# Kernel optimization log

Measured on AMD Instinct MI355X. Metric: run time of the kernel, lower is better.

Reference implementation:

```python
import jax, jax.numpy as jnp
import numpy as np

B, S, HID, NH = 2, 2048, 2048, 16
NOPE, ROPE, VD = 128, 64, 128
QKD = NOPE + ROPE          # 192
KVR, QR = 512, 1536
EPS = 1e-6
SCALE = QKD ** (-0.5)


def rmsnorm(x, gamma, eps=EPS):
    return x * jax.lax.rsqrt(jnp.mean(x * x, axis=-1, keepdims=True) + eps) * gamma


def rotate_half(x):
    h = x.shape[-1] // 2
    return jnp.concatenate([-x[..., h:], x[..., :h]], axis=-1)


def apply_rope(x, cos, sin):
    # x: [b, h, s, d_rope]; cos/sin: [b, 1, s, d_rope]
    return x * cos + rotate_half(x) * sin


def setup_inputs() -> dict:
    key = jax.random.key(0)
    ks = jax.random.split(key, 8)
    hidden_states = jax.random.normal(ks[0], (B, S, HID), dtype=jnp.float32)
    # Standard NeoX-style rotary tables for the decoupled RoPE sub-dim
    pos = jnp.arange(S, dtype=jnp.float32)
    inv_freq = 1.0 / (10000.0 ** (jnp.arange(0, ROPE, 2, dtype=jnp.float32) / ROPE))
    freqs = pos[:, None] * inv_freq[None, :]              # [S, ROPE/2]
    emb = jnp.concatenate([freqs, freqs], axis=-1)        # [S, ROPE]
    cos = jnp.broadcast_to(jnp.cos(emb)[None], (B, S, ROPE)).astype(jnp.float32)
    sin = jnp.broadcast_to(jnp.sin(emb)[None], (B, S, ROPE)).astype(jnp.float32)
    std = 0.02
    Wq_down = jax.random.normal(ks[1], (QR, HID), dtype=jnp.float32) * std
    q_gamma = jnp.ones((QR,), dtype=jnp.float32)
    Wq_up = jax.random.normal(ks[2], (NH * QKD, QR), dtype=jnp.float32) * std
    Wkv_down = jax.random.normal(ks[3], (KVR + ROPE, HID), dtype=jnp.float32) * std
    kv_gamma = jnp.ones((KVR,), dtype=jnp.float32)
    Wkv_up = jax.random.normal(ks[4], (NH * (NOPE + VD), KVR), dtype=jnp.float32) * std
    Wo = jax.random.normal(ks[5], (HID, NH * VD), dtype=jnp.float32) * std
    return {
        "hidden_states": hidden_states, "cos": cos, "sin": sin,
        "Wq_down": Wq_down, "q_gamma": q_gamma, "Wq_up": Wq_up,
        "Wkv_down": Wkv_down, "kv_gamma": kv_gamma, "Wkv_up": Wkv_up,
        "Wo": Wo,
    }


def reference(hidden_states, cos, sin, Wq_down, q_gamma, Wq_up,
              Wkv_down, kv_gamma, Wkv_up, Wo):
    b, s, _ = hidden_states.shape
    cos4 = cos[:, None, :, :]  # [b,1,s,ROPE]
    sin4 = sin[:, None, :, :]

    # Q path: low-rank down -> RMSNorm -> up
    q_lat = rmsnorm(hidden_states @ Wq_down.T, q_gamma)            # [b,s,QR]
    q = (q_lat @ Wq_up.T).reshape(b, s, NH, QKD).transpose(0, 2, 1, 3)  # [b,h,s,QKD]
    q_nope, q_rope = q[..., :NOPE], q[..., NOPE:]
    q_rope = apply_rope(q_rope, cos4, sin4)
    q = jnp.concatenate([q_nope, q_rope], axis=-1)                 # [b,h,s,QKD]

    # KV path: joint down-proj -> split latent / shared rope key
    kv = hidden_states @ Wkv_down.T                                # [b,s,KVR+ROPE]
    c_kv, k_rope = kv[..., :KVR], kv[..., KVR:]
    c_kv = rmsnorm(c_kv, kv_gamma)
    kvx = (c_kv @ Wkv_up.T).reshape(b, s, NH, NOPE + VD).transpose(0, 2, 1, 3)
    k_nope, v = kvx[..., :NOPE], kvx[..., NOPE:]                   # [b,h,s,*]

    # Shared rope key, broadcast to all heads, rotated
    k_rope = apply_rope(k_rope[:, None, :, :], cos4, sin4)         # [b,1,s,ROPE]
    k_rope = jnp.broadcast_to(k_rope, (b, NH, s, ROPE))
    k = jnp.concatenate([k_nope, k_rope], axis=-1)                 # [b,h,s,QKD]

    # SDPA with causal mask (V zero-padded to QKD in the original -> identical
    # to using V directly and slicing, so we use V directly)
    scores = jnp.einsum('bhqd,bhkd->bhqk', q, k) * SCALE           # [b,h,s,s]
    causal = jnp.tril(jnp.ones((s, s), dtype=bool))
    scores = jnp.where(causal[None, None], scores, jnp.finfo(scores.dtype).min)
    attn = jax.nn.softmax(scores, axis=-1)
    out = jnp.einsum('bhqk,bhkd->bhqd', attn, v)                   # [b,h,s,VD]
    out = out.transpose(0, 2, 1, 3).reshape(b, s, NH * VD)
    return out @ Wo.T                                              # [b,s,HID]
```

## Files before the change

### kernel.cpp

```cpp
#include <hip/hip_runtime.h>
#include <math.h>

#define SCALE_F 0.0721687836487032f

typedef __attribute__((ext_vector_type(8))) short bf16x8;
typedef __attribute__((ext_vector_type(4))) float f32x4;
typedef __attribute__((ext_vector_type(4))) unsigned short u16x4;

static __device__ __forceinline__ short f2bf(float f) {
  unsigned u = __float_as_uint(f);
  u += 0x7fffu + ((u >> 16) & 1u);
  return (short)(u >> 16);
}

static __device__ __forceinline__ void gl_lds16(const void* g, void* l) {
  __builtin_amdgcn_global_load_lds((const __attribute__((address_space(1))) void*)g,
                                   (__attribute__((address_space(3))) void*)l, 16, 0, 0);
}

template <int MODE>
__global__ __launch_bounds__(256) void gemm_mfma(
    const short* __restrict__ A, const short* __restrict__ W,
    void* __restrict__ Cout, int N, int K,
    const float* __restrict__ cosb, const float* __restrict__ sinb,
    short* __restrict__ out2)
{
  __shared__ __align__(16) short As[128 * 32];
  __shared__ __align__(16) short Ws[128 * 32];
  const int tid = threadIdx.x;
  const int lane = tid & 63;
  const int quad = lane >> 4, n16 = lane & 15;
  const int bm = blockIdx.y * 128, bn = blockIdx.x * 128;
  const int wr = ((tid >> 6) >> 1) * 64, wc = ((tid >> 6) & 1) * 64;

  f32x4 acc[4][4];
  #pragma unroll
  for (int i = 0; i < 4; ++i)
    #pragma unroll
    for (int j = 0; j < 4; ++j) acc[i][j] = (f32x4){0.f, 0.f, 0.f, 0.f};

  const int r0 = tid >> 2, c0 = (tid & 3) * 8;
  const short* a0p = A + (size_t)(bm + r0) * K + c0;
  const short* a1p = A + (size_t)(bm + 64 + r0) * K + c0;
  const short* w0p = W + (size_t)(bn + r0) * K + c0;
  const short* w1p = W + (size_t)(bn + 64 + r0) * K + c0;
  short* asd0 = &As[tid * 8];
  short* asd1 = &As[2048 + tid * 8];
  short* wsd0 = &Ws[tid * 8];
  short* wsd1 = &Ws[2048 + tid * 8];

  for (int k0 = 0; k0 < K; k0 += 32) {
    gl_lds16(a0p, asd0);
    gl_lds16(a1p, asd1);
    gl_lds16(w0p, wsd0);
    gl_lds16(w1p, wsd1);
    a0p += 32; a1p += 32; w0p += 32; w1p += 32;
    __syncthreads();

    bf16x8 af[4], wf[4];
    #pragma unroll
    for (int i = 0; i < 4; ++i) {
      af[i] = *(const bf16x8*)&As[(wr + i * 16 + n16) * 32 + quad * 8];
      wf[i] = *(const bf16x8*)&Ws[(wc + i * 16 + n16) * 32 + quad * 8];
    }
    #pragma unroll
    for (int i = 0; i < 4; ++i)
      #pragma unroll
      for (int j = 0; j < 4; ++j)
        acc[i][j] = __builtin_amdgcn_mfma_f32_16x16x32_bf16(af[i], wf[j], acc[i][j], 0, 0, 0);
    __syncthreads();
  }

  if (MODE == 0) {
    #pragma unroll
    for (int i = 0; i < 4; ++i)
      #pragma unroll
      for (int r = 0; r < 4; ++r) {
        size_t row = (size_t)(bm + wr + i * 16 + quad * 4 + r);
        #pragma unroll
        for (int j = 0; j < 4; ++j)
          ((float*)Cout)[row * N + bn + wc + j * 16 + n16] = acc[i][j][r];
      }
  } else if (MODE == 2) {
    #pragma unroll
    for (int i = 0; i < 4; ++i)
      #pragma unroll
      for (int r = 0; r < 4; ++r) {
        int m = bm + wr + i * 16 + quad * 4 + r;
        int bb = m >> 11, s = m & 2047;
        #pragma unroll
        for (int j = 0; j < 4; ++j) {
          int col = bn + wc + j * 16 + n16;
          int h = col / 192, c = col - h * 192;
          float v = acc[i][j][r];
          if (c >= 128) {
            int jr = c - 128;
            float part = acc[i][j ^ 2][r];
            float cs = cosb[(size_t)m * 64 + jr], sn = sinb[(size_t)m * 64 + jr];
            v = (jr < 32) ? (v * cs - part * sn) : (v * cs + part * sn);
          }
          ((short*)Cout)[(((size_t)(bb * 16 + h)) * 2048 + s) * 192 + c] = f2bf(v * SCALE_F);
        }
      }
  } else {
    #pragma unroll
    for (int i = 0; i < 4; ++i)
      #pragma unroll
      for (int r = 0; r < 4; ++r) {
        int m = bm + wr + i * 16 + quad * 4 + r;
        int bb = m >> 11, s = m & 2047;
        #pragma unroll
        for (int j = 0; j < 4; ++j) {
          int col = bn + wc + j * 16 + n16;
          int h = col >> 8, c = col & 255;
          short v = f2bf(acc[i][j][r]);
          if (c < 128)
            ((short*)Cout)[(((size_t)(bb * 16 + h)) * 2048 + s) * 192 + c] = v;
          else
            out2[((size_t)(bb * 16 + h) * 128 + (c - 128)) * 2048 + s] = v;
        }
      }
  }
}

__global__ __launch_bounds__(256) void cast_all(
    const float* __restrict__ hidden, const float* __restrict__ Wqd,
    const float* __restrict__ Wqu, const float* __restrict__ Wkvu,
    const float* __restrict__ Wo, const float* __restrict__ Wkvd,
    short* __restrict__ hb, short* __restrict__ Wqd_b, short* __restrict__ Wqu_b,
    short* __restrict__ Wkvu_b, short* __restrict__ Wo_b, short* __restrict__ Wkvd_b)
{
  int blk = blockIdx.x;
  const float* src; short* dst; int i;
  if (blk < 8192)       { src = hidden; dst = hb;     i = (blk * 256 + threadIdx.x) * 4; }
  else if (blk < 11264) { src = Wqd;  dst = Wqd_b;  i = ((blk - 8192) * 256 + threadIdx.x) * 4; }
  else if (blk < 15872) { src = Wqu;  dst = Wqu_b;  i = ((blk - 11264) * 256 + threadIdx.x) * 4; }
  else if (blk < 17920) { src = Wkvu; dst = Wkvu_b; i = ((blk - 15872) * 256 + threadIdx.x) * 4; }
  else if (blk < 22016) { src = Wo;   dst = Wo_b;   i = ((blk - 17920) * 256 + threadIdx.x) * 4; }
  else {
    i = ((blk - 22016) * 256 + threadIdx.x) * 4;
    int r = i >> 11;
    short4 o = {0, 0, 0, 0};
    if (r < 576) {
      float4 v = *(const float4*)(Wkvd + i);
      o.x = f2bf(v.x); o.y = f2bf(v.y); o.z = f2bf(v.z); o.w = f2bf(v.w);
    }
    *(short4*)(Wkvd_b + i) = o;
    return;
  }
  float4 v = *(const float4*)(src + i);
  short4 o = { f2bf(v.x), f2bf(v.y), f2bf(v.z), f2bf(v.w) };
  *(short4*)(dst + i) = o;
}

__global__ __launch_bounds__(256) void rmsnorm_cast(
    const float* __restrict__ X, const float* __restrict__ gamma,
    short* __restrict__ Y, int C, int sx, int sy)
{
  const float* x = X + (size_t)blockIdx.x * sx;
  short* y = Y + (size_t)blockIdx.x * sy;
  const int tid = threadIdx.x;
  float ss = 0.f;
  for (int c = tid * 4; c < C; c += 1024) {
    float4 v = *(const float4*)(x + c);
    ss += v.x * v.x + v.y * v.y + v.z * v.z + v.w * v.w;
  }
  #pragma unroll
  for (int off = 32; off > 0; off >>= 1) ss += __shfl_down(ss, off, 64);
  __shared__ float red[4];
  if ((tid & 63) == 0) red[tid >> 6] = ss;
  __syncthreads();
  float tot = red[0] + red[1] + red[2] + red[3];
  float scale = rsqrtf(tot / (float)C + 1e-6f);
  for (int c = tid * 4; c < C; c += 1024) {
    float4 v = *(const float4*)(x + c);
    float4 g = *(const float4*)(gamma + c);
    short4 o = { f2bf(v.x * scale * g.x), f2bf(v.y * scale * g.y),
                 f2bf(v.z * scale * g.z), f2bf(v.w * scale * g.w) };
    *(short4*)(y + c) = o;
  }
}

__global__ __launch_bounds__(256) void rmsnorm_kv_rope(
    const float* __restrict__ kvf, const float* __restrict__ gamma,
    const float* __restrict__ cosb, const float* __restrict__ sinb,
    short* __restrict__ ckv, short* __restrict__ kr)
{
  const int m = blockIdx.x;
  const float* x = kvf + (size_t)m * 640;
  short* y = ckv + (size_t)m * 512;
  const int tid = threadIdx.x;
  float ss = 0.f;
  for (int c = tid * 4; c < 512; c += 1024) {
    float4 v = *(const float4*)(x + c);
    ss += v.x * v.x + v.y * v.y + v.z * v.z + v.w * v.w;
  }
  #pragma unroll
  for (int off = 32; off > 0; off >>= 1) ss += __shfl_down(ss, off, 64);
  __shared__ float red[4];
  if ((tid & 63) == 0) red[tid >> 6] = ss;
  __syncthreads();
  float tot = red[0] + red[1] + red[2] + red[3];
  float scale = rsqrtf(tot / 512.f + 1e-6f);
  for (int c = tid * 4; c < 512; c += 1024) {
    float4 v = *(const float4*)(x + c);
    float4 g = *(const float4*)(gamma + c);
    short4 o = { f2bf(v.x * scale * g.x), f2bf(v.y * scale * g.y),
                 f2bf(v.z * scale * g.z), f2bf(v.w * scale * g.w) };
    *(short4*)(y + c) = o;
  }
  if (tid < 32) {
    const float* cb = cosb + (size_t)m * 64;
    const float* sb = sinb + (size_t)m * 64;
    float x1 = x[512 + tid], x2 = x[512 + tid + 32];
    kr[(size_t)m * 64 + tid]      = f2bf(x1 * cb[tid] - x2 * sb[tid]);
    kr[(size_t)m * 64 + tid + 32] = f2bf(x2 * cb[tid + 32] + x1 * sb[tid + 32]);
  }
}

__global__ __launch_bounds__(256) void krope_fill(
    const short* __restrict__ kr, short* __restrict__ Kb)
{
  int m = blockIdx.x;
  int b = m >> 11, s = m & 2047;
  for (int idx = threadIdx.x; idx < 1024; idx += 256) {
    int h = idx >> 6, j = idx & 63;
    Kb[(((size_t)(b * 16 + h)) * 2048 + s) * 192 + 128 + j] = kr[(size_t)m * 64 + j];
  }
}

#define PSTR 72

__global__ __launch_bounds__(256, 2) void flash_mfma(
    const short* __restrict__ Qb, const short* __restrict__ Kb,
    const short* __restrict__ Vt, short* __restrict__ attnb)
{
  __shared__ __align__(16) short KsF[24 * 512];
  __shared__ __align__(16) short VsF[16 * 512];
  __shared__ __align__(16) short Ps[4][32 * PSTR];

  const int h = blockIdx.x;
  const int qt = (gridDim.y - 1) - blockIdx.y;
  const int b = blockIdx.z;
  const int bh = b * 16 + h;
  const int tid = threadIdx.x;
  const int wave = tid >> 6, lane = tid & 63;
  const int quad = lane >> 4, n16 = lane & 15;
  const int lq = lane >> 2, lr = lane & 3;
  const int qw = qt * 128 + wave * 32;
  const int nkt = 2 * qt + 2;

  bf16x8 aQ[2][6];
  #pragma unroll
  for (int rg = 0; rg < 2; ++rg) {
    const short* qp = Qb + ((size_t)bh * 2048 + qw + rg * 16 + n16) * 192 + quad * 8;
    #pragma unroll
    for (int t = 0; t < 6; ++t) aQ[rg][t] = *(const bf16x8*)(qp + t * 32);
  }

  f32x4 O[2][8];
  #pragma unroll
  for (int rg = 0; rg < 2; ++rg)
    #pragma unroll
    for (int i = 0; i < 8; ++i) O[rg][i] = (f32x4){0.f, 0.f, 0.f, 0.f};
  float lp[2] = {0.f, 0.f};

  short* pw = &Ps[wave][0];

  for (int kt = 0; kt < nkt; ++kt) {
    {
      const short* kbase = Kb + ((size_t)bh * 2048 + kt * 64 + wave * 16 + lq) * 192 + lr * 8;
      #pragma unroll
      for (int u = 0; u < 6; ++u)
        gl_lds16(kbase + u * 32, &KsF[(wave * 6 + u) * 512 + lane * 8]);
      #pragma unroll
      for (int u = 0; u < 4; ++u) {
        int ci = wave * 4 + u, ks = ci >> 3, vt = ci & 7;
        gl_lds16(Vt + ((size_t)bh * 128 + vt * 16 + lq) * 2048 + kt * 64 + ks * 32 + lr * 8,
                 &VsF[ci * 512 + lane * 8]);
      }
    }
    __syncthreads();

    if (kt * 64 <= qw + 31) {
      float s[4][2][4];
      bool act[4];
      const bool tail = (kt * 64 + 63 > qw);
      #pragma unroll
      for (int ct = 0; ct < 4; ++ct) {
        act[ct] = (kt * 64 + ct * 16 <= qw + 31);
        if (act[ct]) {
          f32x4 a0 = (f32x4){0.f, 0.f, 0.f, 0.f};
          f32x4 a1 = (f32x4){0.f, 0.f, 0.f, 0.f};
          #pragma unroll
          for (int t = 0; t < 6; ++t) {
            bf16x8 ak = *(const bf16x8*)&KsF[(ct * 6 + t) * 512 + n16 * 32 + quad * 8];
            a0 = __builtin_amdgcn_mfma_f32_16x16x32_bf16(ak, aQ[0][t], a0, 0, 0, 0);
            a1 = __builtin_amdgcn_mfma_f32_16x16x32_bf16(ak, aQ[1][t], a1, 0, 0, 0);
          }
          #pragma unroll
          for (int r = 0; r < 4; ++r) { s[ct][0][r] = a0[r]; s[ct][1][r] = a1[r]; }
        }
      }

      #pragma unroll
      for (int rg = 0; rg < 2; ++rg) {
        const int q = qw + rg * 16 + n16;
        #pragma unroll
        for (int ct = 0; ct < 4; ++ct) {
          u16x4 pk;
          #pragma unroll
          for (int r = 0; r < 4; ++r) {
            float v = 0.f;
            if (act[ct]) {
              v = __expf(s[ct][rg][r]);
              if (tail) {
                int key = kt * 64 + ct * 16 + quad * 4 + r;
                if (key > q) v = 0.f;
              }
            }
            lp[rg] += v;
            pk[r] = (unsigned short)f2bf(v);
          }
          *(u16x4*)&pw[(rg * 16 + n16) * PSTR + ct * 16 + quad * 4] = pk;
        }
      }

      #pragma unroll
      for (int ks = 0; ks < 2; ++ks) {
        if (kt * 64 + ks * 32 <= qw + 31) {
          bf16x8 aP0 = *(const bf16x8*)&pw[(n16) * PSTR + ks * 32 + quad * 8];
          bf16x8 aP1 = *(const bf16x8*)&pw[(16 + n16) * PSTR + ks * 32 + quad * 8];
          #pragma unroll
          for (int vt = 0; vt < 8; ++vt) {
            bf16x8 bV = *(const bf16x8*)&VsF[(ks * 8 + vt) * 512 + n16 * 32 + quad * 8];
            O[0][vt] = __builtin_amdgcn_mfma_f32_16x16x32_bf16(aP0, bV, O[0][vt], 0, 0, 0);
            O[1][vt] = __builtin_amdgcn_mfma_f32_16x16x32_bf16(aP1, bV, O[1][vt], 0, 0, 0);
          }
        }
      }
    }
    __syncthreads();
  }

  #pragma unroll
  for (int rg = 0; rg < 2; ++rg) {
    float l = lp[rg];
    l += __shfl_xor(l, 16);
    l += __shfl_xor(l, 32);
    float inv_l[4];
    #pragma unroll
    for (int r = 0; r < 4; ++r)
      inv_l[r] = 1.f / __shfl(l, quad * 4 + r);
    #pragma unroll
    for (int vt = 0; vt < 8; ++vt)
      #pragma unroll
      for (int r = 0; r < 4; ++r) {
        size_t m = (size_t)b * 2048 + qw + rg * 16 + quad * 4 + r;
        attnb[(m * 16 + h) * 128 + vt * 16 + n16] = f2bf(O[rg][vt][r] * inv_l[r]);
      }
  }
}

extern "C" void kernel_launch(void* const* d_in, const int* in_sizes, int n_in,
                              void* d_out, int out_size, void* d_ws, size_t ws_size,
                              hipStream_t stream)
{
  const float* hidden   = (const float*)d_in[0];
  const float* cosb     = (const float*)d_in[1];
  const float* sinb     = (const float*)d_in[2];
  const float* Wq_down  = (const float*)d_in[3];
  const float* q_gamma  = (const float*)d_in[4];
  const float* Wq_up    = (const float*)d_in[5];
  const float* Wkv_down = (const float*)d_in[6];
  const float* kv_gamma = (const float*)d_in[7];
  const float* Wkv_up   = (const float*)d_in[8];
  const float* Wo       = (const float*)d_in[9];
  float* out = (float*)d_out;

  char* base = (char*)d_ws;
  short* hb  = (short*)base;
  float* kvf = (float*)(base + 16777216);
  short* Qb  = (short*)base;
  char* pB = base + 27262976;
  short* Wqd_b  = (short*)pB;
  short* Wkvd_b = (short*)(pB + 6291456);
  short* Wqu_b  = (short*)(pB + 8912896);
  short* Wkvu_b = (short*)(pB + 18350080);
  short* Wo_b   = (short*)(pB + 22544384);
  char* pC = pB + 30932992;
  float* q_lat = (float*)pC;
  short* Kb    = (short*)pC;
  char* pD = pC + 25165824;
  short* q_lat_b = (short*)pD;
  short* ckv_b   = (short*)(pD + 12582912);
  short* krope_b = (short*)(pD + 16777216);
  short* attn_b  = (short*)pD;
  char* pE = pD + 17301504;
  short* Vt = (short*)pE;

  dim3 blk(256);

  cast_all<<<23296, blk, 0, stream>>>(hidden, Wq_down, Wq_up, Wkv_up, Wo, Wkv_down,
                                      hb, Wqd_b, Wqu_b, Wkvu_b, Wo_b, Wkvd_b);

  gemm_mfma<0><<<dim3(12, 32), blk, 0, stream>>>(hb, Wqd_b, q_lat, 1536, 2048, nullptr, nullptr, nullptr);
  gemm_mfma<0><<<dim3(5, 32), blk, 0, stream>>>(hb, Wkvd_b, kvf, 640, 2048, nullptr, nullptr, nullptr);

  rmsnorm_cast<<<4096, blk, 0, stream>>>(q_lat, q_gamma, q_lat_b, 1536, 1536, 1536);
  rmsnorm_kv_rope<<<4096, blk, 0, stream>>>(kvf, kv_gamma, cosb, sinb, ckv_b, krope_b);

  gemm_mfma<2><<<dim3(24, 32), blk, 0, stream>>>(q_lat_b, Wqu_b, Qb, 3072, 1536, cosb, sinb, nullptr);
  gemm_mfma<3><<<dim3(32, 32), blk, 0, stream>>>(ckv_b, Wkvu_b, Kb, 4096, 512, nullptr, nullptr, Vt);
  krope_fill<<<4096, blk, 0, stream>>>(krope_b, Kb);

  flash_mfma<<<dim3(16, 16, 2), blk, 0, stream>>>(Qb, Kb, Vt, attn_b);
  gemm_mfma<0><<<dim3(16, 32), blk, 0, stream>>>(attn_b, Wo_b, out, 2048, 2048, nullptr, nullptr, nullptr);
}
```

Before: 541.8 us.

## Use two-wave flash blocks with 64 query rows per wave; transpose V separately

The flash attention kernel now runs 128 threads per block, and each wave handles 64 query rows instead of 32. Each K/V tile loaded into LDS is therefore reused across more MFMA work per wave, at the cost of many more registers and less occupancy. The KV-up GEMM epilogue now writes V row-major with coalesced stores, and a new LDS-tiled transpose kernel builds the transposed V layout that flash attention expects. This replaces the previous strided scattered stores but adds an extra kernel and an extra pass over V in memory.

```diff
diff --git a/kernel.cpp b/kernel.cpp
--- a/kernel.cpp
+++ b/kernel.cpp
@@ -117,7 +117,7 @@
           if (c < 128)
             ((short*)Cout)[(((size_t)(bb * 16 + h)) * 2048 + s) * 192 + c] = v;
           else
-            out2[((size_t)(bb * 16 + h) * 128 + (c - 128)) * 2048 + s] = v;
+            out2[((size_t)(bb * 16 + h) * 2048 + s) * 128 + (c - 128)] = v;
         }
       }
   }
@@ -229,15 +229,34 @@
   }
 }
 
+__global__ __launch_bounds__(256) void pack_vt(
+    const short* __restrict__ Vrow, short* __restrict__ Vt)
+{
+  __shared__ short t[32][34];
+  int s0 = blockIdx.x * 32, v0 = blockIdx.y * 32, bh = blockIdx.z;
+  int c = threadIdx.x & 31, r4 = threadIdx.x >> 5;
+  #pragma unroll
+  for (int rr = 0; rr < 32; rr += 8) {
+    int s = s0 + rr + r4;
+    t[rr + r4][c] = Vrow[((size_t)bh * 2048 + s) * 128 + v0 + c];
+  }
+  __syncthreads();
+  #pragma unroll
+  for (int rr = 0; rr < 32; rr += 8) {
+    int v = v0 + rr + r4;
+    Vt[((size_t)bh * 128 + v) * 2048 + s0 + c] = t[c][rr + r4];
+  }
+}
+
 #define PSTR 72
 
-__global__ __launch_bounds__(256, 2) void flash_mfma(
+__global__ __launch_bounds__(128, 1) void flash_mfma(
     const short* __restrict__ Qb, const short* __restrict__ Kb,
     const short* __restrict__ Vt, short* __restrict__ attnb)
 {
   __shared__ __align__(16) short KsF[24 * 512];
   __shared__ __align__(16) short VsF[16 * 512];
-  __shared__ __align__(16) short Ps[4][32 * PSTR];
+  __shared__ __align__(16) short Ps[2][32 * PSTR];
 
   const int h = blockIdx.x;
   const int qt = (gridDim.y - 1) - blockIdx.y;
@@ -247,104 +266,109 @@
   const int wave = tid >> 6, lane = tid & 63;
   const int quad = lane >> 4, n16 = lane & 15;
   const int lq = lane >> 2, lr = lane & 3;
-  const int qw = qt * 128 + wave * 32;
+  const int qw = qt * 128 + wave * 64;
   const int nkt = 2 * qt + 2;
 
-  bf16x8 aQ[2][6];
-  #pragma unroll
-  for (int rg = 0; rg < 2; ++rg) {
+  bf16x8 aQ[4][6];
+  #pragma unroll
+  for (int rg = 0; rg < 4; ++rg) {
     const short* qp = Qb + ((size_t)bh * 2048 + qw + rg * 16 + n16) * 192 + quad * 8;
     #pragma unroll
     for (int t = 0; t < 6; ++t) aQ[rg][t] = *(const bf16x8*)(qp + t * 32);
   }
 
-  f32x4 O[2][8];
-  #pragma unroll
-  for (int rg = 0; rg < 2; ++rg)
+  f32x4 O[4][8];
+  #pragma unroll
+  for (int rg = 0; rg < 4; ++rg)
     #pragma unroll
     for (int i = 0; i < 8; ++i) O[rg][i] = (f32x4){0.f, 0.f, 0.f, 0.f};
-  float lp[2] = {0.f, 0.f};
+  float lp[4] = {0.f, 0.f, 0.f, 0.f};
 
   short* pw = &Ps[wave][0];
 
   for (int kt = 0; kt < nkt; ++kt) {
     {
-      const short* kbase = Kb + ((size_t)bh * 2048 + kt * 64 + wave * 16 + lq) * 192 + lr * 8;
-      #pragma unroll
-      for (int u = 0; u < 6; ++u)
-        gl_lds16(kbase + u * 32, &KsF[(wave * 6 + u) * 512 + lane * 8]);
-      #pragma unroll
-      for (int u = 0; u < 4; ++u) {
-        int ci = wave * 4 + u, ks = ci >> 3, vt = ci & 7;
+      #pragma unroll
+      for (int u = 0; u < 12; ++u) {
+        int ci = wave * 12 + u, ct = ci / 6, t = ci % 6;
+        gl_lds16(Kb + ((size_t)bh * 2048 + kt * 64 + ct * 16 + lq) * 192 + t * 32 + lr * 8,
+                 &KsF[ci * 512 + lane * 8]);
+      }
+      #pragma unroll
+      for (int u = 0; u < 8; ++u) {
+        int ci = wave * 8 + u, ks = ci >> 3, vt = ci & 7;
         gl_lds16(Vt + ((size_t)bh * 128 + vt * 16 + lq) * 2048 + kt * 64 + ks * 32 + lr * 8,
                  &VsF[ci * 512 + lane * 8]);
       }
     }
     __syncthreads();
 
-    if (kt * 64 <= qw + 31) {
-      float s[4][2][4];
+    if (kt * 64 <= qw + 63) {
+      const bool tail = (kt * 64 + 63 > qw);
       bool act[4];
-      const bool tail = (kt * 64 + 63 > qw);
+      f32x4 s4[4][4];
       #pragma unroll
       for (int ct = 0; ct < 4; ++ct) {
-        act[ct] = (kt * 64 + ct * 16 <= qw + 31);
+        act[ct] = (kt * 64 + ct * 16 <= qw + 63);
         if (act[ct]) {
-          f32x4 a0 = (f32x4){0.f, 0.f, 0.f, 0.f};
-          f32x4 a1 = (f32x4){0.f, 0.f, 0.f, 0.f};
+          f32x4 a0 = (f32x4){0.f,0.f,0.f,0.f}, a1 = a0, a2 = a0, a3 = a0;
           #pragma unroll
           for (int t = 0; t < 6; ++t) {
             bf16x8 ak = *(const bf16x8*)&KsF[(ct * 6 + t) * 512 + n16 * 32 + quad * 8];
             a0 = __builtin_amdgcn_mfma_f32_16x16x32_bf16(ak, aQ[0][t], a0, 0, 0, 0);
             a1 = __builtin_amdgcn_mfma_f32_16x16x32_bf16(ak, aQ[1][t], a1, 0, 0, 0);
+            a2 = __builtin_amdgcn_mfma_f32_16x16x32_bf16(ak, aQ[2][t], a2, 0, 0, 0);
+            a3 = __builtin_amdgcn_mfma_f32_16x16x32_bf16(ak, aQ[3][t], a3, 0, 0, 0);
           }
+          s4[0][ct] = a0; s4[1][ct] = a1; s4[2][ct] = a2; s4[3][ct] = a3;
+        }
+      }
+
+      #pragma unroll
+      for (int p = 0; p < 2; ++p) {
+        #pragma unroll
+        for (int rgl = 0; rgl < 2; ++rgl) {
+          const int rg = p * 2 + rgl;
+          const int q = qw + rg * 16 + n16;
           #pragma unroll
-          for (int r = 0; r < 4; ++r) { s[ct][0][r] = a0[r]; s[ct][1][r] = a1[r]; }
-        }
-      }
-
-      #pragma unroll
-      for (int rg = 0; rg < 2; ++rg) {
-        const int q = qw + rg * 16 + n16;
-        #pragma unroll
-        for (int ct = 0; ct < 4; ++ct) {
-          u16x4 pk;
-          #pragma unroll
-          for (int r = 0; r < 4; ++r) {
-            float v = 0.f;
-            if (act[ct]) {
-              v = __expf(s[ct][rg][r]);
-              if (tail) {
-                int key = kt * 64 + ct * 16 + quad * 4 + r;
-                if (key > q) v = 0.f;
+          for (int ct = 0; ct < 4; ++ct) {
+            u16x4 pk;
+            #pragma unroll
+            for (int r = 0; r < 4; ++r) {
+              float v = 0.f;
+              if (act[ct]) {
+                v = __expf(s4[rg][ct][r]);
+                if (tail) {
+                  int key = kt * 64 + ct * 16 + quad * 4 + r;
+                  if (key > q) v = 0.f;
+                }
               }
+              lp[rg] += v;
+              pk[r] = (unsigned short)f2bf(v);
             }
-            lp[rg] += v;
-            pk[r] = (unsigned short)f2bf(v);
-          }
-          *(u16x4*)&pw[(rg * 16 + n16) * PSTR + ct * 16 + quad * 4] = pk;
-        }
-      }
-
-      #pragma unroll
-      for (int ks = 0; ks < 2; ++ks) {
-        if (kt * 64 + ks * 32 <= qw + 31) {
-          bf16x8 aP0 = *(const bf16x8*)&pw[(n16) * PSTR + ks * 32 + quad * 8];
-          bf16x8 aP1 = *(const bf16x8*)&pw[(16 + n16) * PSTR + ks * 32 + quad * 8];
-          #pragma unroll
-          for (int vt = 0; vt < 8; ++vt) {
-            bf16x8 bV = *(const bf16x8*)&VsF[(ks * 8 + vt) * 512 + n16 * 32 + quad * 8];
-            O[0][vt] = __builtin_amdgcn_mfma_f32_16x16x32_bf16(aP0, bV, O[0][vt], 0, 0, 0);
-            O[1][vt] = __builtin_amdgcn_mfma_f32_16x16x32_bf16(aP1, bV, O[1][vt], 0, 0, 0);
+            *(u16x4*)&pw[(rgl * 16 + n16) * PSTR + ct * 16 + quad * 4] = pk;
           }
         }
+        #pragma unroll
+        for (int ks = 0; ks < 2; ++ks) {
+          if (kt * 64 + ks * 32 <= qw + 63) {
+            bf16x8 aP0 = *(const bf16x8*)&pw[(n16) * PSTR + ks * 32 + quad * 8];
+            bf16x8 aP1 = *(const bf16x8*)&pw[(16 + n16) * PSTR + ks * 32 + quad * 8];
+            #pragma unroll
+            for (int vt = 0; vt < 8; ++vt) {
+              bf16x8 bV = *(const bf16x8*)&VsF[(ks * 8 + vt) * 512 + n16 * 32 + quad * 8];
+              O[p * 2][vt]     = __builtin_amdgcn_mfma_f32_16x16x32_bf16(aP0, bV, O[p * 2][vt], 0, 0, 0);
+              O[p * 2 + 1][vt] = __builtin_amdgcn_mfma_f32_16x16x32_bf16(aP1, bV, O[p * 2 + 1][vt], 0, 0, 0);
+            }
+          }
+        }
       }
     }
     __syncthreads();
   }
 
   #pragma unroll
-  for (int rg = 0; rg < 2; ++rg) {
+  for (int rg = 0; rg < 4; ++rg) {
     float l = lp[rg];
     l += __shfl_xor(l, 16);
     l += __shfl_xor(l, 32);
@@ -397,7 +421,8 @@
   short* krope_b = (short*)(pD + 16777216);
   short* attn_b  = (short*)pD;
   char* pE = pD + 17301504;
-  short* Vt = (short*)pE;
+  short* Vt   = (short*)pE;
+  short* Vrow = (short*)(pE + 16777216);
 
   dim3 blk(256);
 
@@ -411,9 +436,10 @@
   rmsnorm_kv_rope<<<4096, blk, 0, stream>>>(kvf, kv_gamma, cosb, sinb, ckv_b, krope_b);
 
   gemm_mfma<2><<<dim3(24, 32), blk, 0, stream>>>(q_lat_b, Wqu_b, Qb, 3072, 1536, cosb, sinb, nullptr);
-  gemm_mfma<3><<<dim3(32, 32), blk, 0, stream>>>(ckv_b, Wkvu_b, Kb, 4096, 512, nullptr, nullptr, Vt);
+  gemm_mfma<3><<<dim3(32, 32), blk, 0, stream>>>(ckv_b, Wkvu_b, Kb, 4096, 512, nullptr, nullptr, Vrow);
+  pack_vt<<<dim3(64, 4, 32), blk, 0, stream>>>(Vrow, Vt);
   krope_fill<<<4096, blk, 0, stream>>>(krope_b, Kb);
 
-  flash_mfma<<<dim3(16, 16, 2), blk, 0, stream>>>(Qb, Kb, Vt, attn_b);
+  flash_mfma<<<dim3(16, 16, 2), dim3(128), 0, stream>>>(Qb, Kb, Vt, attn_b);
   gemm_mfma<0><<<dim3(16, 32), blk, 0, stream>>>(attn_b, Wo_b, out, 2048, 2048, nullptr, nullptr, nullptr);
 }
```

New measurement: 587.9 us. 8.5% more time.
